# Optimization experiments

Hardware: AMD Instinct MI355X
Metric: run time of the kernel (lower is better)

## Reference

```python
import jax, jax.numpy as jnp
import numpy as np

B, T, S, H, V = 4, 512, 1024, 768, 50257

def setup_inputs() -> dict:
    key = jax.random.key(0)
    k1, k2, k3, k4, k5, k6 = jax.random.split(key, 6)
    input_ids_to_copy = jax.random.randint(k1, (B, S), 0, V)
    cross_attentions = jax.random.uniform(k2, (B, T, S), dtype=jnp.float32)
    # normalize like attention weights
    cross_attentions = cross_attentions / jnp.sum(cross_attentions, axis=-1, keepdims=True)
    src_hidden_states = jax.random.normal(k3, (B, S, H), dtype=jnp.float32)
    tgt_hidden_states = jax.random.normal(k4, (B, T, H), dtype=jnp.float32)
    # p_gen_head = Linear(2H, 1) + Sigmoid
    W_pgen = jax.random.normal(k5, (2 * H, 1), dtype=jnp.float32) * (1.0 / np.sqrt(2 * H))
    b_pgen = jnp.zeros((1,), dtype=jnp.float32)
    return {
        "input_ids_to_copy": input_ids_to_copy,
        "cross_attentions": cross_attentions,
        "src_hidden_states": src_hidden_states,
        "tgt_hidden_states": tgt_hidden_states,
        "W_pgen": W_pgen,
        "b_pgen": b_pgen,
    }

def _copy_logits(attn_bts, ids_bs, vocab_size):
    # logits[b,t,v] = sum_s attn[b,t,s] * (ids[b,s] == v)
    # Efficient scatter-add over source positions instead of one-hot + matmul.
    def per_batch(attn_ts, ids_s):
        # attn_ts: [T,S], ids_s: [S] -> segment_sum over S -> [V,T] -> [T,V]
        return jax.ops.segment_sum(attn_ts.T, ids_s, num_segments=vocab_size).T
    return jax.vmap(per_batch)(attn_bts, ids_bs)

def reference(input_ids_to_copy, cross_attentions, src_hidden_states,
              tgt_hidden_states, W_pgen, b_pgen):
    # context_vectors: [B,T,H]
    context_vectors = jnp.einsum('bts,bsh->bth', cross_attentions, src_hidden_states)
    total_states = jnp.concatenate((context_vectors, tgt_hidden_states), axis=-1)  # [B,T,2H]
    p_gen = jax.nn.sigmoid(total_states @ W_pgen + b_pgen)  # [B,T,1]
    logits = _copy_logits(cross_attentions, input_ids_to_copy, V)  # [B,T,V]
    return (p_gen, logits)
```

## Files before the change

### kernel.cpp

```cpp
#include <hip/hip_runtime.h>
#include <hip/hip_bf16.h>
#include <math.h>

#define BB 4
#define TT 512
#define SS 1024
#define HH 768
#define VV 50257
#define NW 1571
#define NWP 1600
#define NPROJ 1536

__global__ __launch_bounds__(256) void prep_kernel(
    const float* __restrict__ src, const float* __restrict__ tgt,
    const float* __restrict__ W, const float* __restrict__ bptr,
    const int* __restrict__ ids,
    float* __restrict__ src_proj, float* __restrict__ tgt_proj,
    unsigned* __restrict__ bm_g, unsigned* __restrict__ pre_g,
    unsigned short* __restrict__ rank_g)
{
    __shared__ unsigned bm[NW];
    __shared__ unsigned pre[NW];
    __shared__ unsigned scan[256];
    const int tid = threadIdx.x;

    if (blockIdx.x < NPROJ) {
        const int wave = tid >> 6;
        const int lane = tid & 63;
        const int row  = blockIdx.x * 4 + wave;

        const float* vec;
        const float* w;
        if (row < BB * SS) { vec = src + (size_t)row * HH;            w = W; }
        else               { vec = tgt + (size_t)(row - BB*SS) * HH;  w = W + HH; }
        const float4* v4 = (const float4*)vec;
        const float4* w4 = (const float4*)w;

        float acc = 0.f;
#pragma unroll
        for (int k = 0; k < 3; ++k) {
            float4 a = v4[k * 64 + lane];
            float4 b = w4[k * 64 + lane];
            acc += a.x * b.x + a.y * b.y + a.z * b.z + a.w * b.w;
        }
#pragma unroll
        for (int off = 32; off > 0; off >>= 1) acc += __shfl_down(acc, off);
        if (lane == 0) {
            if (row < BB * SS) src_proj[row] = acc;
            else               tgt_proj[row - BB * SS] = acc + bptr[0];
        }
        return;
    }

    const int b = blockIdx.x - NPROJ;

    for (int i = tid; i < NW; i += 256) bm[i] = 0u;
    __syncthreads();
    const int* idb = ids + b * SS;
    for (int s = tid; s < SS; s += 256) {
        const int v = idb[s];
        atomicOr(&bm[v >> 5], 1u << (v & 31));
    }
    __syncthreads();

    unsigned cnt[7];
    unsigned local = 0;
    const int w0 = tid * 7;
#pragma unroll
    for (int k = 0; k < 7; ++k) {
        const int w = w0 + k;
        cnt[k] = local;
        local += (w < NW) ? (unsigned)__popc(bm[w]) : 0u;
    }
    scan[tid] = local;
    __syncthreads();
    for (int off = 1; off < 256; off <<= 1) {
        const unsigned mine = scan[tid];
        const unsigned add  = (tid >= off) ? scan[tid - off] : 0u;
        __syncthreads();
        scan[tid] = mine + add;
        __syncthreads();
    }
    const unsigned excl = (tid > 0) ? scan[tid - 1] : 0u;
#pragma unroll
    for (int k = 0; k < 7; ++k) {
        const int w = w0 + k;
        if (w < NW) {
            const unsigned p = excl + cnt[k];
            pre[w] = p;
            pre_g[b * NWP + w] = p;
            bm_g[b * NWP + w]  = bm[w];
        }
    }
    __syncthreads();
    for (int s = tid; s < SS; s += 256) {
        const int v = idb[s];
        const unsigned w = (unsigned)v >> 5, bit = (unsigned)v & 31u;
        const unsigned r = pre[w] + (unsigned)__popc(bm[w] & ((1u << bit) - 1u));
        rank_g[b * SS + s] = (unsigned short)r;
    }
}

__device__ __forceinline__ float lut1(int v, const unsigned* bm,
                                      const unsigned* pre, const float* vals)
{
    const unsigned w = bm[v >> 5];
    const unsigned bit = (unsigned)v & 31u;
    if ((w >> bit) & 1u)
        return vals[pre[v >> 5] + (unsigned)__popc(w & ((1u << bit) - 1u))];
    return 0.f;
}

__global__ __launch_bounds__(256) void row_kernel(
    const float* __restrict__ attn,
    const float* __restrict__ src_proj,
    const float* __restrict__ tgt_proj,
    const unsigned* __restrict__ bm_g,
    const unsigned* __restrict__ pre_g,
    const unsigned short* __restrict__ rank_g,
    float* __restrict__ out)
{
    __shared__ unsigned bm[NW];
    __shared__ unsigned pre[NW];
    __shared__ float vals[SS];
    __shared__ float wsum[4];

    const int row = blockIdx.x;
    const int b   = row >> 9;
    const int tid = threadIdx.x;

    for (int i = tid; i < NW; i += 256) { bm[i] = bm_g[b*NWP+i]; pre[i] = pre_g[b*NWP+i]; }
    ((float4*)vals)[tid] = make_float4(0.f, 0.f, 0.f, 0.f);
    __syncthreads();

    const float4*  a4p = (const float4*)(attn + (size_t)row * SS);
    const float4*  sp4 = (const float4*)(src_proj + b * SS);
    const ushort4* r4p = (const ushort4*)(rank_g + b * SS);
    const float4  a = a4p[tid];
    const float4  p = sp4[tid];
    const ushort4 r = r4p[tid];
    atomicAdd(&vals[r.x], a.x);
    atomicAdd(&vals[r.y], a.y);
    atomicAdd(&vals[r.z], a.z);
    atomicAdd(&vals[r.w], a.w);
    float acc = a.x * p.x + a.y * p.y + a.z * p.z + a.w * p.w;
#pragma unroll
    for (int off = 32; off > 0; off >>= 1) acc += __shfl_down(acc, off);
    if ((tid & 63) == 0) wsum[tid >> 6] = acc;
    __syncthreads();
    if (tid == 0) {
        const float x = wsum[0] + wsum[1] + wsum[2] + wsum[3] + tgt_proj[row];
        out[row] = 1.f / (1.f + expf(-x));
    }

    float* logits = out + (BB * TT) + (size_t)row * VV;
    const int head = (int)(((16u - (unsigned)((uintptr_t)logits & 15u)) & 15u) >> 2);
    if (tid < head) logits[tid] = lut1(tid, bm, pre, vals);

    const int n4 = (VV - head) >> 2;
    float4* p4 = (float4*)(logits + head);
    for (int i = tid; i < n4; i += 256) {
        const int v0 = head + (i << 2);
        float4 o = make_float4(0.f, 0.f, 0.f, 0.f);
        const unsigned w  = bm[v0 >> 5];
        const unsigned sh = (unsigned)v0 & 31u;
        unsigned nib;
        if (sh <= 28u) {
            nib = (w >> sh) & 0xFu;
        } else {
            const unsigned hi = bm[(v0 >> 5) + 1];
            nib = ((w >> sh) | (hi << (32u - sh))) & 0xFu;
        }
        if (nib) {
            o.x = lut1(v0,     bm, pre, vals);
            o.y = lut1(v0 + 1, bm, pre, vals);
            o.z = lut1(v0 + 2, bm, pre, vals);
            o.w = lut1(v0 + 3, bm, pre, vals);
        }
        p4[i] = o;
    }
    const int done = head + (n4 << 2);
    for (int v = done + tid; v < VV; v += 256)
        logits[v] = lut1(v, bm, pre, vals);
}

extern "C" void kernel_launch(void* const* d_in, const int* in_sizes, int n_in,
                              void* d_out, int out_size, void* d_ws, size_t ws_size,
                              hipStream_t stream) {
    const int*   ids  = (const int*)d_in[0];
    const float* attn = (const float*)d_in[1];
    const float* src  = (const float*)d_in[2];
    const float* tgt  = (const float*)d_in[3];
    const float* W    = (const float*)d_in[4];
    const float* bp   = (const float*)d_in[5];

    float* out = (float*)d_out;

    float*          src_proj = (float*)d_ws;
    float*          tgt_proj = src_proj + BB * SS;
    unsigned*       bm_g     = (unsigned*)(tgt_proj + BB * TT);
    unsigned*       pre_g    = bm_g + BB * NWP;
    unsigned short* rank_g   = (unsigned short*)(pre_g + BB * NWP);

    prep_kernel<<<NPROJ + BB, 256, 0, stream>>>(
        src, tgt, W, bp, ids, src_proj, tgt_proj, bm_g, pre_g, rank_g);
    row_kernel<<<BB * TT, 256, 0, stream>>>(
        attn, src_proj, tgt_proj, bm_g, pre_g, rank_g, out);
}
```

Measured before the change: 465.6 us.

## Split logits writes into sparse dirty-line pass and zero-fill pass

Prep now builds, for each of the four possible row alignments, a bitmap of 64-byte output lines that contain any copied token, plus a compact list of those lines. The row kernel first writes the nonzero lines from the list using the LUT, then writes zero float4s only to lines not in the bitmap. This removes the per-float4 bitmap nibble test and LUT branches from the dense store loop, leaving it as a near-pure zero store. The cost is extra prep work, more workspace, and a second scattered store pass.

Result: slower. 583.7 us (+25.4%).

```diff
diff --git a/kernel.cpp b/kernel.cpp
--- a/kernel.cpp
+++ b/kernel.cpp
@@ -10,6 +10,7 @@
 #define NW 1571
 #define NWP 1600
 #define NPROJ 1536
+#define NLB 128
 
 __global__ __launch_bounds__(256) void prep_kernel(
     const float* __restrict__ src, const float* __restrict__ tgt,
@@ -17,11 +18,14 @@
     const int* __restrict__ ids,
     float* __restrict__ src_proj, float* __restrict__ tgt_proj,
     unsigned* __restrict__ bm_g, unsigned* __restrict__ pre_g,
-    unsigned short* __restrict__ rank_g)
+    unsigned* __restrict__ lbm_g, unsigned* __restrict__ dllc_g,
+    unsigned short* __restrict__ rank_g, unsigned short* __restrict__ dll_g)
 {
     __shared__ unsigned bm[NW];
     __shared__ unsigned pre[NW];
     __shared__ unsigned scan[256];
+    __shared__ unsigned lbm[4 * NLB];
+    __shared__ unsigned dcnt[4];
     const int tid = threadIdx.x;
 
     if (blockIdx.x < NPROJ) {
@@ -99,6 +103,40 @@
         const unsigned r = pre[w] + (unsigned)__popc(bm[w] & ((1u << bit) - 1u));
         rank_g[b * SS + s] = (unsigned short)r;
     }
+
+    for (int i = tid; i < 4 * NLB; i += 256) lbm[i] = 0u;
+    if (tid < 4) dcnt[tid] = 0u;
+    __syncthreads();
+    for (int s = tid; s < SS; s += 256) {
+        const int v = idb[s];
+#pragma unroll
+        for (int h = 0; h < 4; ++h) {
+            if (v >= h) {
+                const int m = (v - h) >> 4;
+                atomicOr(&lbm[(h << 7) + (m >> 5)], 1u << (m & 31));
+            }
+        }
+    }
+    __syncthreads();
+    for (int w = tid; w < 4 * NLB; w += 256) {
+        const unsigned word = lbm[w];
+        const int h  = w >> 7;
+        const int wi = w & (NLB - 1);
+        lbm_g[(b * 4 + h) * NLB + wi] = word;
+        if (word) {
+            const int n = __popc(word);
+            unsigned base = atomicAdd(&dcnt[h], (unsigned)n);
+            unsigned x = word;
+            while (x) {
+                const int bit = __ffs(x) - 1;
+                dll_g[(size_t)(b * 4 + h) * 1024 + base++] =
+                    (unsigned short)((wi << 5) + bit);
+                x &= x - 1u;
+            }
+        }
+    }
+    __syncthreads();
+    if (tid < 4) dllc_g[b * 4 + tid] = dcnt[tid];
 }
 
 __device__ __forceinline__ float lut1(int v, const unsigned* bm,
@@ -117,19 +155,27 @@
     const float* __restrict__ tgt_proj,
     const unsigned* __restrict__ bm_g,
     const unsigned* __restrict__ pre_g,
+    const unsigned* __restrict__ lbm_g,
+    const unsigned* __restrict__ dllc_g,
     const unsigned short* __restrict__ rank_g,
+    const unsigned short* __restrict__ dll_g,
     float* __restrict__ out)
 {
     __shared__ unsigned bm[NW];
     __shared__ unsigned pre[NW];
     __shared__ float vals[SS];
     __shared__ float wsum[4];
+    __shared__ unsigned lbm_s[NLB];
 
     const int row = blockIdx.x;
     const int b   = row >> 9;
     const int tid = threadIdx.x;
 
+    float* logits = out + (BB * TT) + (size_t)row * VV;
+    const int head = (int)(((16u - (unsigned)((uintptr_t)logits & 15u)) & 15u) >> 2);
+
     for (int i = tid; i < NW; i += 256) { bm[i] = bm_g[b*NWP+i]; pre[i] = pre_g[b*NWP+i]; }
+    if (tid < NLB) lbm_s[tid] = lbm_g[(b * 4 + head) * NLB + tid];
     ((float4*)vals)[tid] = make_float4(0.f, 0.f, 0.f, 0.f);
     __syncthreads();
 
@@ -153,32 +199,33 @@
         out[row] = 1.f / (1.f + expf(-x));
     }
 
-    float* logits = out + (BB * TT) + (size_t)row * VV;
-    const int head = (int)(((16u - (unsigned)((uintptr_t)logits & 15u)) & 15u) >> 2);
-    if (tid < head) logits[tid] = lut1(tid, bm, pre, vals);
-
     const int n4 = (VV - head) >> 2;
     float4* p4 = (float4*)(logits + head);
-    for (int i = tid; i < n4; i += 256) {
-        const int v0 = head + (i << 2);
-        float4 o = make_float4(0.f, 0.f, 0.f, 0.f);
-        const unsigned w  = bm[v0 >> 5];
-        const unsigned sh = (unsigned)v0 & 31u;
-        unsigned nib;
-        if (sh <= 28u) {
-            nib = (w >> sh) & 0xFu;
-        } else {
-            const unsigned hi = bm[(v0 >> 5) + 1];
-            nib = ((w >> sh) | (hi << (32u - sh))) & 0xFu;
-        }
-        if (nib) {
+
+    const int dn = (int)dllc_g[b * 4 + head];
+    const unsigned short* dll = dll_g + (size_t)(b * 4 + head) * 1024;
+    for (int j = tid; j < dn * 4; j += 256) {
+        const int m = (int)dll[j >> 2];
+        const int g = (m << 2) + (j & 3);
+        if (g < n4) {
+            const int v0 = head + (g << 2);
+            float4 o;
             o.x = lut1(v0,     bm, pre, vals);
             o.y = lut1(v0 + 1, bm, pre, vals);
             o.z = lut1(v0 + 2, bm, pre, vals);
             o.w = lut1(v0 + 3, bm, pre, vals);
-        }
-        p4[i] = o;
-    }
+            p4[g] = o;
+        }
+    }
+
+    const float4 z4 = make_float4(0.f, 0.f, 0.f, 0.f);
+    for (int i = tid; i < n4; i += 256) {
+        const int line = i >> 2;
+        if (!((lbm_s[line >> 5] >> (line & 31)) & 1u))
+            p4[i] = z4;
+    }
+
+    if (tid < head) logits[tid] = lut1(tid, bm, pre, vals);
     const int done = head + (n4 << 2);
     for (int v = done + tid; v < VV; v += 256)
         logits[v] = lut1(v, bm, pre, vals);
@@ -200,10 +247,15 @@
     float*          tgt_proj = src_proj + BB * SS;
     unsigned*       bm_g     = (unsigned*)(tgt_proj + BB * TT);
     unsigned*       pre_g    = bm_g + BB * NWP;
-    unsigned short* rank_g   = (unsigned short*)(pre_g + BB * NWP);
+    unsigned*       lbm_g    = pre_g + BB * NWP;
+    unsigned*       dllc_g   = lbm_g + BB * 4 * NLB;
+    unsigned short* rank_g   = (unsigned short*)(dllc_g + 16);
+    unsigned short* dll_g    = rank_g + BB * SS;
 
     prep_kernel<<<NPROJ + BB, 256, 0, stream>>>(
-        src, tgt, W, bp, ids, src_proj, tgt_proj, bm_g, pre_g, rank_g);
+        src, tgt, W, bp, ids, src_proj, tgt_proj, bm_g, pre_g,
+        lbm_g, dllc_g, rank_g, dll_g);
     row_kernel<<<BB * TT, 256, 0, stream>>>(
-        attn, src_proj, tgt_proj, bm_g, pre_g, rank_g, out);
-}
+        attn, src_proj, tgt_proj, bm_g, pre_g, lbm_g, dllc_g,
+        rank_g, dll_g, out);
+}
```

## Process two output rows per block with interleaved bitmap/prefix table and float2 values

Applied to the files above, without the earlier changes.

The row kernel now handles pairs of consecutive target rows per block (with edge rows alone), so the per-batch bitmap/prefix tables are loaded into LDS once per pair instead of once per row. The bitmap and prefix arrays are interleaved as uint2, and the scattered values are stored as float2 so one lookup serves both rows. The pair's two rows have complementary alignment offsets, so both get aligned float4 stores from one 5-bit window. This cuts LDS setup and lookup work per row at the cost of more complex indexing and fewer blocks.

Result: no change. 465.6 us (-0.0%).

```diff
diff --git a/kernel.cpp b/kernel.cpp
--- a/kernel.cpp
+++ b/kernel.cpp
@@ -1,5 +1,4 @@
 #include <hip/hip_runtime.h>
-#include <hip/hip_bf16.h>
 #include <math.h>
 
 #define BB 4
@@ -10,14 +9,14 @@
 #define NW 1571
 #define NWP 1600
 #define NPROJ 1536
+#define KPB 257
 
 __global__ __launch_bounds__(256) void prep_kernel(
     const float* __restrict__ src, const float* __restrict__ tgt,
     const float* __restrict__ W, const float* __restrict__ bptr,
     const int* __restrict__ ids,
     float* __restrict__ src_proj, float* __restrict__ tgt_proj,
-    unsigned* __restrict__ bm_g, unsigned* __restrict__ pre_g,
-    unsigned short* __restrict__ rank_g)
+    uint2* __restrict__ bmpre_g, unsigned short* __restrict__ rank_g)
 {
     __shared__ unsigned bm[NW];
     __shared__ unsigned pre[NW];
@@ -88,10 +87,10 @@
         if (w < NW) {
             const unsigned p = excl + cnt[k];
             pre[w] = p;
-            pre_g[b * NWP + w] = p;
-            bm_g[b * NWP + w]  = bm[w];
-        }
-    }
+            bmpre_g[b * NWP + w] = make_uint2(bm[w], p);
+        }
+    }
+    if (tid == 0) bmpre_g[b * NWP + NW] = make_uint2(0u, 0u);
     __syncthreads();
     for (int s = tid; s < SS; s += 256) {
         const int v = idb[s];
@@ -101,87 +100,138 @@
     }
 }
 
-__device__ __forceinline__ float lut1(int v, const unsigned* bm,
-                                      const unsigned* pre, const float* vals)
+__device__ __forceinline__ float2 lut2(int u, const uint2* __restrict__ bmpre,
+                                       const float2* __restrict__ vals2)
 {
-    const unsigned w = bm[v >> 5];
-    const unsigned bit = (unsigned)v & 31u;
-    if ((w >> bit) & 1u)
-        return vals[pre[v >> 5] + (unsigned)__popc(w & ((1u << bit) - 1u))];
-    return 0.f;
-}
+    const uint2 bp = bmpre[u >> 5];
+    const unsigned bt = (unsigned)u & 31u;
+    if ((bp.x >> bt) & 1u)
+        return vals2[bp.y + (unsigned)__popc(bp.x & ((1u << bt) - 1u))];
+    return make_float2(0.f, 0.f);
+}
+
+#define ELEM(J, DST)                                                        \
+    if (m5 & (1u << (J))) {                                                 \
+        const unsigned t  = (unsigned)s + (J);                              \
+        const unsigned bw = (t >= 32u) ? bp1.x : bp0.x;                     \
+        const unsigned pw = (t >= 32u) ? bp1.y : bp0.y;                     \
+        const unsigned bt = t & 31u;                                        \
+        DST = vals2[pw + (unsigned)__popc(bw & ((1u << bt) - 1u))];         \
+    }
 
 __global__ __launch_bounds__(256) void row_kernel(
     const float* __restrict__ attn,
     const float* __restrict__ src_proj,
     const float* __restrict__ tgt_proj,
-    const unsigned* __restrict__ bm_g,
-    const unsigned* __restrict__ pre_g,
+    const uint2* __restrict__ bmpre_g,
     const unsigned short* __restrict__ rank_g,
     float* __restrict__ out)
 {
-    __shared__ unsigned bm[NW];
-    __shared__ unsigned pre[NW];
-    __shared__ float vals[SS];
-    __shared__ float wsum[4];
-
-    const int row = blockIdx.x;
-    const int b   = row >> 9;
-    const int tid = threadIdx.x;
-
-    for (int i = tid; i < NW; i += 256) { bm[i] = bm_g[b*NWP+i]; pre[i] = pre_g[b*NWP+i]; }
-    ((float4*)vals)[tid] = make_float4(0.f, 0.f, 0.f, 0.f);
-    __syncthreads();
-
-    const float4*  a4p = (const float4*)(attn + (size_t)row * SS);
-    const float4*  sp4 = (const float4*)(src_proj + b * SS);
-    const ushort4* r4p = (const ushort4*)(rank_g + b * SS);
-    const float4  a = a4p[tid];
-    const float4  p = sp4[tid];
-    const ushort4 r = r4p[tid];
-    atomicAdd(&vals[r.x], a.x);
-    atomicAdd(&vals[r.y], a.y);
-    atomicAdd(&vals[r.z], a.z);
-    atomicAdd(&vals[r.w], a.w);
-    float acc = a.x * p.x + a.y * p.y + a.z * p.z + a.w * p.w;
-#pragma unroll
-    for (int off = 32; off > 0; off >>= 1) acc += __shfl_down(acc, off);
-    if ((tid & 63) == 0) wsum[tid >> 6] = acc;
+    __shared__ uint2  bmpre[NW + 1];
+    __shared__ float2 vals2[SS];
+    __shared__ float  wsa[4], wsb[4];
+
+    const int tid   = threadIdx.x;
+    const int bid   = blockIdx.x;
+    const int batch = bid / KPB;
+    const int k     = bid - batch * KPB;
+    const bool pair = (k > 0) && (k < 256);
+    int row_a;
+    if (k == 0)        row_a = batch * TT;
+    else if (k == 256) row_a = batch * TT + 511;
+    else               row_a = batch * TT + 2 * k - 1;
+    const int row_b = pair ? row_a + 1 : row_a;
+
+    for (int i = tid; i < NW + 1; i += 256) bmpre[i] = bmpre_g[batch * NWP + i];
+    ((float4*)vals2)[tid]       = make_float4(0.f, 0.f, 0.f, 0.f);
+    ((float4*)vals2)[tid + 256] = make_float4(0.f, 0.f, 0.f, 0.f);
+    __syncthreads();
+
+    const float4*  aA  = (const float4*)(attn + (size_t)row_a * SS);
+    const float4*  aB  = (const float4*)(attn + (size_t)row_b * SS);
+    const float4*  sp4 = (const float4*)(src_proj + batch * SS);
+    const ushort4* r4p = (const ushort4*)(rank_g + batch * SS);
+    const float4  va = aA[tid];
+    const float4  p  = sp4[tid];
+    const ushort4 r  = r4p[tid];
+    atomicAdd(&vals2[r.x].x, va.x);
+    atomicAdd(&vals2[r.y].x, va.y);
+    atomicAdd(&vals2[r.z].x, va.z);
+    atomicAdd(&vals2[r.w].x, va.w);
+    float accA = va.x * p.x + va.y * p.y + va.z * p.z + va.w * p.w;
+    float accB = 0.f;
+    if (pair) {
+        const float4 vb = aB[tid];
+        atomicAdd(&vals2[r.x].y, vb.x);
+        atomicAdd(&vals2[r.y].y, vb.y);
+        atomicAdd(&vals2[r.z].y, vb.z);
+        atomicAdd(&vals2[r.w].y, vb.w);
+        accB = vb.x * p.x + vb.y * p.y + vb.z * p.z + vb.w * p.w;
+    }
+#pragma unroll
+    for (int off = 32; off > 0; off >>= 1) {
+        accA += __shfl_down(accA, off);
+        accB += __shfl_down(accB, off);
+    }
+    if ((tid & 63) == 0) { wsa[tid >> 6] = accA; wsb[tid >> 6] = accB; }
     __syncthreads();
     if (tid == 0) {
-        const float x = wsum[0] + wsum[1] + wsum[2] + wsum[3] + tgt_proj[row];
-        out[row] = 1.f / (1.f + expf(-x));
-    }
-
-    float* logits = out + (BB * TT) + (size_t)row * VV;
-    const int head = (int)(((16u - (unsigned)((uintptr_t)logits & 15u)) & 15u) >> 2);
-    if (tid < head) logits[tid] = lut1(tid, bm, pre, vals);
-
-    const int n4 = (VV - head) >> 2;
-    float4* p4 = (float4*)(logits + head);
-    for (int i = tid; i < n4; i += 256) {
-        const int v0 = head + (i << 2);
-        float4 o = make_float4(0.f, 0.f, 0.f, 0.f);
-        const unsigned w  = bm[v0 >> 5];
-        const unsigned sh = (unsigned)v0 & 31u;
-        unsigned nib;
-        if (sh <= 28u) {
-            nib = (w >> sh) & 0xFu;
-        } else {
-            const unsigned hi = bm[(v0 >> 5) + 1];
-            nib = ((w >> sh) | (hi << (32u - sh))) & 0xFu;
-        }
-        if (nib) {
-            o.x = lut1(v0,     bm, pre, vals);
-            o.y = lut1(v0 + 1, bm, pre, vals);
-            o.z = lut1(v0 + 2, bm, pre, vals);
-            o.w = lut1(v0 + 3, bm, pre, vals);
-        }
-        p4[i] = o;
-    }
-    const int done = head + (n4 << 2);
-    for (int v = done + tid; v < VV; v += 256)
-        logits[v] = lut1(v, bm, pre, vals);
+        const float x = wsa[0] + wsa[1] + wsa[2] + wsa[3] + tgt_proj[row_a];
+        out[row_a] = 1.f / (1.f + expf(-x));
+    }
+    if (pair && tid == 1) {
+        const float x = wsb[0] + wsb[1] + wsb[2] + wsb[3] + tgt_proj[row_b];
+        out[row_b] = 1.f / (1.f + expf(-x));
+    }
+
+    float* la = out + (BB * TT) + (size_t)row_a * VV;
+    const int h = (4 - (row_a & 3)) & 3;
+    const int n = (VV - h) >> 2;
+
+    if (pair) {
+        float* lb = la + VV;
+        for (int i = tid; i < n; i += 256) {
+            const int v = h + (i << 2);
+            const int s = (v - 1) & 31;
+            const int w = (v - 1) >> 5;
+            const uint2 bp0 = bmpre[w];
+            const uint2 bp1 = bmpre[w + 1];
+            unsigned m5 = bp0.x >> s;
+            if (s >= 28) m5 |= (bp1.x << (32 - s));
+            m5 &= 31u;
+            float2 e0 = make_float2(0.f, 0.f), e1 = e0, e2 = e0, e3 = e0, e4 = e0;
+            if (m5) {
+                ELEM(0, e0) ELEM(1, e1) ELEM(2, e2) ELEM(3, e3) ELEM(4, e4)
+            }
+            *(float4*)(la + v)     = make_float4(e1.x, e2.x, e3.x, e4.x);
+            *(float4*)(lb + v - 1) = make_float4(e0.y, e1.y, e2.y, e3.y);
+        }
+        if (tid < h)     la[tid] = lut2(tid, bmpre, vals2).x;
+        if (tid < h - 1) lb[tid] = lut2(tid, bmpre, vals2).y;
+        const int ta = h + (n << 2);
+        if (ta + tid < VV) la[ta + tid] = lut2(ta + tid, bmpre, vals2).x;
+        const int tb = (h - 1) + (n << 2);
+        if (tb + tid < VV) lb[tb + tid] = lut2(tb + tid, bmpre, vals2).y;
+    } else {
+        for (int i = tid; i < n; i += 256) {
+            const int v = h + (i << 2);
+            const int s = v & 31;
+            const int w = v >> 5;
+            const uint2 bp0 = bmpre[w];
+            const uint2 bp1 = bmpre[w + 1];
+            unsigned m5 = bp0.x >> s;
+            if (s >= 29) m5 |= (bp1.x << (32 - s));
+            m5 &= 15u;
+            float2 e0 = make_float2(0.f, 0.f), e1 = e0, e2 = e0, e3 = e0;
+            if (m5) {
+                ELEM(0, e0) ELEM(1, e1) ELEM(2, e2) ELEM(3, e3)
+            }
+            *(float4*)(la + v) = make_float4(e0.x, e1.x, e2.x, e3.x);
+        }
+        if (tid < h) la[tid] = lut2(tid, bmpre, vals2).x;
+        const int ta = h + (n << 2);
+        if (ta + tid < VV) la[ta + tid] = lut2(ta + tid, bmpre, vals2).x;
+    }
 }
 
 extern "C" void kernel_launch(void* const* d_in, const int* in_sizes, int n_in,
@@ -198,12 +248,11 @@
 
     float*          src_proj = (float*)d_ws;
     float*          tgt_proj = src_proj + BB * SS;
-    unsigned*       bm_g     = (unsigned*)(tgt_proj + BB * TT);
-    unsigned*       pre_g    = bm_g + BB * NWP;
-    unsigned short* rank_g   = (unsigned short*)(pre_g + BB * NWP);
+    uint2*          bmpre_g  = (uint2*)(tgt_proj + BB * TT);
+    unsigned short* rank_g   = (unsigned short*)(bmpre_g + BB * NWP);
 
     prep_kernel<<<NPROJ + BB, 256, 0, stream>>>(
-        src, tgt, W, bp, ids, src_proj, tgt_proj, bm_g, pre_g, rank_g);
-    row_kernel<<<BB * TT, 256, 0, stream>>>(
-        attn, src_proj, tgt_proj, bm_g, pre_g, rank_g, out);
-}
+        src, tgt, W, bp, ids, src_proj, tgt_proj, bmpre_g, rank_g);
+    row_kernel<<<BB * KPB, 256, 0, stream>>>(
+        attn, src_proj, tgt_proj, bmpre_g, rank_g, out);
+}
```

## Split logits write into separate flat grid-stride sweep over compact per-row values

Applied to the files above, without the earlier changes.

The per-row kernel is split in two. A value kernel scatters attention into compact per-row rank buffers and writes them to workspace. A separate sweep kernel then writes the whole flat logits array with aligned float4 stores in a grid-stride loop, using interleaved bitmap/prefix pairs held in shared memory. The intent is to turn the dominant ~412MB zero-heavy output write into a flat, aligned stream that does not pay per-row setup and misaligned head/tail handling. The cost is an extra launch, an 8MB intermediate round trip, and a per-element integer division.

After: 475.0 us. 1.02x slower.

```diff
diff --git a/kernel.cpp b/kernel.cpp
--- a/kernel.cpp
+++ b/kernel.cpp
@@ -1,5 +1,4 @@
 #include <hip/hip_runtime.h>
-#include <hip/hip_bf16.h>
 #include <math.h>
 
 #define BB 4
@@ -10,14 +9,17 @@
 #define NW 1571
 #define NWP 1600
 #define NPROJ 1536
+#define NROWS (BB * TT)
+#define NV (NROWS * VV)
+#define NG (NV / 4)
+#define K2_GRID 768
 
 __global__ __launch_bounds__(256) void prep_kernel(
     const float* __restrict__ src, const float* __restrict__ tgt,
     const float* __restrict__ W, const float* __restrict__ bptr,
     const int* __restrict__ ids,
     float* __restrict__ src_proj, float* __restrict__ tgt_proj,
-    unsigned* __restrict__ bm_g, unsigned* __restrict__ pre_g,
-    unsigned short* __restrict__ rank_g)
+    uint2* __restrict__ bmpre_g, unsigned short* __restrict__ rank_g)
 {
     __shared__ unsigned bm[NW];
     __shared__ unsigned pre[NW];
@@ -88,10 +90,10 @@
         if (w < NW) {
             const unsigned p = excl + cnt[k];
             pre[w] = p;
-            pre_g[b * NWP + w] = p;
-            bm_g[b * NWP + w]  = bm[w];
-        }
-    }
+            bmpre_g[b * NWP + w] = make_uint2(bm[w], p);
+        }
+    }
+    if (tid == 0) bmpre_g[b * NWP + NW] = make_uint2(0u, 0u);
     __syncthreads();
     for (int s = tid; s < SS; s += 256) {
         const int v = idb[s];
@@ -101,44 +103,26 @@
     }
 }
 
-__device__ __forceinline__ float lut1(int v, const unsigned* bm,
-                                      const unsigned* pre, const float* vals)
-{
-    const unsigned w = bm[v >> 5];
-    const unsigned bit = (unsigned)v & 31u;
-    if ((w >> bit) & 1u)
-        return vals[pre[v >> 5] + (unsigned)__popc(w & ((1u << bit) - 1u))];
-    return 0.f;
-}
-
-__global__ __launch_bounds__(256) void row_kernel(
+__global__ __launch_bounds__(256) void val_kernel(
     const float* __restrict__ attn,
     const float* __restrict__ src_proj,
     const float* __restrict__ tgt_proj,
-    const unsigned* __restrict__ bm_g,
-    const unsigned* __restrict__ pre_g,
     const unsigned short* __restrict__ rank_g,
+    float* __restrict__ dval,
     float* __restrict__ out)
 {
-    __shared__ unsigned bm[NW];
-    __shared__ unsigned pre[NW];
     __shared__ float vals[SS];
     __shared__ float wsum[4];
-
     const int row = blockIdx.x;
     const int b   = row >> 9;
     const int tid = threadIdx.x;
 
-    for (int i = tid; i < NW; i += 256) { bm[i] = bm_g[b*NWP+i]; pre[i] = pre_g[b*NWP+i]; }
     ((float4*)vals)[tid] = make_float4(0.f, 0.f, 0.f, 0.f);
     __syncthreads();
 
-    const float4*  a4p = (const float4*)(attn + (size_t)row * SS);
-    const float4*  sp4 = (const float4*)(src_proj + b * SS);
-    const ushort4* r4p = (const ushort4*)(rank_g + b * SS);
-    const float4  a = a4p[tid];
-    const float4  p = sp4[tid];
-    const ushort4 r = r4p[tid];
+    const float4  a = ((const float4*)(attn + (size_t)row * SS))[tid];
+    const float4  p = ((const float4*)(src_proj + b * SS))[tid];
+    const ushort4 r = ((const ushort4*)(rank_g + b * SS))[tid];
     atomicAdd(&vals[r.x], a.x);
     atomicAdd(&vals[r.y], a.y);
     atomicAdd(&vals[r.z], a.z);
@@ -148,40 +132,73 @@
     for (int off = 32; off > 0; off >>= 1) acc += __shfl_down(acc, off);
     if ((tid & 63) == 0) wsum[tid >> 6] = acc;
     __syncthreads();
+
+    ((float4*)(dval + ((size_t)row << 10)))[tid] = ((float4*)vals)[tid];
     if (tid == 0) {
         const float x = wsum[0] + wsum[1] + wsum[2] + wsum[3] + tgt_proj[row];
         out[row] = 1.f / (1.f + expf(-x));
     }
-
-    float* logits = out + (BB * TT) + (size_t)row * VV;
-    const int head = (int)(((16u - (unsigned)((uintptr_t)logits & 15u)) & 15u) >> 2);
-    if (tid < head) logits[tid] = lut1(tid, bm, pre, vals);
-
-    const int n4 = (VV - head) >> 2;
-    float4* p4 = (float4*)(logits + head);
-    for (int i = tid; i < n4; i += 256) {
-        const int v0 = head + (i << 2);
-        float4 o = make_float4(0.f, 0.f, 0.f, 0.f);
-        const unsigned w  = bm[v0 >> 5];
-        const unsigned sh = (unsigned)v0 & 31u;
-        unsigned nib;
-        if (sh <= 28u) {
-            nib = (w >> sh) & 0xFu;
+}
+
+#define GELEM(J, DST)                                                       \
+    if (m4 & (1u << (J))) {                                                 \
+        const unsigned t  = (unsigned)s + (J);                              \
+        const unsigned bw = (t >= 32u) ? bp1.x : bp0.x;                     \
+        const unsigned pw = (t >= 32u) ? bp1.y : bp0.y;                     \
+        const unsigned bt = t & 31u;                                        \
+        DST = dvrow[pw + (unsigned)__popc(bw & ((1u << bt) - 1u))];         \
+    }
+
+__global__ __launch_bounds__(256) void sweep_kernel(
+    const uint2* __restrict__ bmpre_g,
+    const float* __restrict__ dval,
+    float* __restrict__ out)
+{
+    __shared__ uint2 bmpre[4 * (NW + 1)];
+    const int tid = threadIdx.x;
+
+    for (int i = tid; i < 4 * (NW + 1); i += 256) {
+        const int b = i / (NW + 1);
+        const int w = i - b * (NW + 1);
+        bmpre[i] = bmpre_g[b * NWP + w];
+    }
+    __syncthreads();
+
+    float* logits = out + NROWS;
+    const int stride = K2_GRID * 256;
+    for (int g = blockIdx.x * 256 + tid; g < NG; g += stride) {
+        const int f0 = g << 2;
+        const unsigned r = (unsigned)f0 / VV;
+        const int v0 = f0 - (int)(r * VV);
+        if (v0 + 3 < VV) {
+            const uint2* bp = bmpre + ((r >> 9) * (NW + 1));
+            const float* dvrow = dval + ((size_t)r << 10);
+            const int s = v0 & 31;
+            const int w = v0 >> 5;
+            const uint2 bp0 = bp[w];
+            const uint2 bp1 = bp[w + 1];
+            unsigned m4 = bp0.x >> s;
+            if (s >= 29) m4 |= (bp1.x << (32 - s));
+            m4 &= 15u;
+            float e0 = 0.f, e1 = 0.f, e2 = 0.f, e3 = 0.f;
+            if (m4) { GELEM(0, e0) GELEM(1, e1) GELEM(2, e2) GELEM(3, e3) }
+            *(float4*)(logits + f0) = make_float4(e0, e1, e2, e3);
         } else {
-            const unsigned hi = bm[(v0 >> 5) + 1];
-            nib = ((w >> sh) | (hi << (32u - sh))) & 0xFu;
-        }
-        if (nib) {
-            o.x = lut1(v0,     bm, pre, vals);
-            o.y = lut1(v0 + 1, bm, pre, vals);
-            o.z = lut1(v0 + 2, bm, pre, vals);
-            o.w = lut1(v0 + 3, bm, pre, vals);
-        }
-        p4[i] = o;
-    }
-    const int done = head + (n4 << 2);
-    for (int v = done + tid; v < VV; v += 256)
-        logits[v] = lut1(v, bm, pre, vals);
+#pragma unroll
+            for (int j = 0; j < 4; ++j) {
+                const int f = f0 + j;
+                const unsigned re = (unsigned)f / VV;
+                const int ve = f - (int)(re * VV);
+                const uint2 bw = bmpre[(re >> 9) * (NW + 1) + (ve >> 5)];
+                const unsigned bt = (unsigned)ve & 31u;
+                float e = 0.f;
+                if ((bw.x >> bt) & 1u)
+                    e = dval[((size_t)re << 10) + bw.y
+                             + (unsigned)__popc(bw.x & ((1u << bt) - 1u))];
+                logits[f] = e;
+            }
+        }
+    }
 }
 
 extern "C" void kernel_launch(void* const* d_in, const int* in_sizes, int n_in,
@@ -198,12 +215,14 @@
 
     float*          src_proj = (float*)d_ws;
     float*          tgt_proj = src_proj + BB * SS;
-    unsigned*       bm_g     = (unsigned*)(tgt_proj + BB * TT);
-    unsigned*       pre_g    = bm_g + BB * NWP;
-    unsigned short* rank_g   = (unsigned short*)(pre_g + BB * NWP);
+    uint2*          bmpre_g  = (uint2*)(tgt_proj + BB * TT);
+    unsigned short* rank_g   = (unsigned short*)(bmpre_g + BB * NWP);
+    float*          dval     = (float*)(rank_g + BB * SS);
 
     prep_kernel<<<NPROJ + BB, 256, 0, stream>>>(
-        src, tgt, W, bp, ids, src_proj, tgt_proj, bm_g, pre_g, rank_g);
-    row_kernel<<<BB * TT, 256, 0, stream>>>(
-        attn, src_proj, tgt_proj, bm_g, pre_g, rank_g, out);
-}
+        src, tgt, W, bp, ids, src_proj, tgt_proj, bmpre_g, rank_g);
+    val_kernel<<<NROWS, 256, 0, stream>>>(
+        attn, src_proj, tgt_proj, rank_g, dval, out);
+    sweep_kernel<<<K2_GRID, 256, 0, stream>>>(
+        bmpre_g, dval, out);
+}
```
